# Kernel optimization log

Measured on AMD Instinct MI355X. Metric: run time of the kernel, lower is better.

The kernel has to match this reference:

```python
import jax, jax.numpy as jnp
import numpy as np

B, S, D = 4, 1024, 2048
H, KVH = 32, 8
HD = D // H            # 64
KVD = HD * KVH         # 512
RANK, ALPHA = 16, 32
LORA_SCALE = ALPHA / RANK


def setup_inputs() -> dict:
    key = jax.random.key(0)
    ks = jax.random.split(key, 14)
    x = jax.random.normal(ks[0], (B, S, D), dtype=jnp.float32)
    # RoPE tables (llama-style complex freqs as cos/sin)
    inv = 1.0 / (10000.0 ** (np.arange(0, HD, 2, dtype=np.float32) / HD))
    t = np.arange(S, dtype=np.float32)
    ang = np.outer(t, inv)  # [S, HD//2]
    freqs_cos = jnp.asarray(np.cos(ang))
    freqs_sin = jnp.asarray(np.sin(ang))
    s = 0.02
    Wq = jax.random.normal(ks[1], (D, D), dtype=jnp.float32) * s
    Wk = jax.random.normal(ks[2], (D, KVD), dtype=jnp.float32) * s
    Wv = jax.random.normal(ks[3], (D, KVD), dtype=jnp.float32) * s
    Wo = jax.random.normal(ks[4], (D, D), dtype=jnp.float32) * s
    qA = jax.random.normal(ks[5], (D, RANK), dtype=jnp.float32) * s
    qB = jax.random.normal(ks[6], (RANK, D), dtype=jnp.float32) * s
    kA = jax.random.normal(ks[7], (D, RANK), dtype=jnp.float32) * s
    kB = jax.random.normal(ks[8], (RANK, KVD), dtype=jnp.float32) * s
    vA = jax.random.normal(ks[9], (D, RANK), dtype=jnp.float32) * s
    vB = jax.random.normal(ks[10], (RANK, KVD), dtype=jnp.float32) * s
    return {"x": x, "freqs_cos": freqs_cos, "freqs_sin": freqs_sin,
            "Wq": Wq, "Wk": Wk, "Wv": Wv, "Wo": Wo,
            "qA": qA, "qB": qB, "kA": kA, "kB": kB, "vA": vA, "vB": vB}


def _rope(t, cos, sin):
    # t: [b, s, h, hd]; cos/sin: [s, hd//2]
    b, s, h, hd = t.shape
    t2 = t.reshape(b, s, h, hd // 2, 2)
    x0, x1 = t2[..., 0], t2[..., 1]
    c = cos[None, :, None, :]
    sn = sin[None, :, None, :]
    r0 = x0 * c - x1 * sn
    r1 = x0 * sn + x1 * c
    return jnp.stack([r0, r1], axis=-1).reshape(b, s, h, hd)


def reference(x, freqs_cos, freqs_sin, Wq, Wk, Wv, Wo, qA, qB, kA, kB, vA, vB):
    b, s, _ = x.shape
    # QKV projections + LoRA deltas
    q = x @ Wq + (x @ qA) @ qB * LORA_SCALE   # [b,s,D]
    k = x @ Wk + (x @ kA) @ kB * LORA_SCALE   # [b,s,KVD]
    v = x @ Wv + (x @ vA) @ vB * LORA_SCALE   # [b,s,KVD]
    q = q.reshape(b, s, H, HD)
    k = k.reshape(b, s, KVH, HD)
    v = v.reshape(b, s, KVH, HD)
    q = _rope(q, freqs_cos, freqs_sin)
    k = _rope(k, freqs_cos, freqs_sin)
    # GQA attention without materializing repeated K/V:
    rep = H // KVH
    qg = q.reshape(b, s, KVH, rep, HD)
    scale = 1.0 / jnp.sqrt(jnp.asarray(HD, dtype=x.dtype))
    scores = jnp.einsum('bsgrd,btgd->bgrst', qg, k) * scale  # [b,kvh,rep,s,s]
    causal = jnp.tril(jnp.ones((s, s), dtype=bool))
    scores = jnp.where(causal[None, None, None], scores, jnp.finfo(scores.dtype).min)
    attn = jax.nn.softmax(scores, axis=-1)
    ctx = jnp.einsum('bgrst,btgd->bsgrd', attn, v).reshape(b, s, D)
    return ctx @ Wo
```

## Files before the change

### kernel.cpp

```cpp
#include <hip/hip_runtime.h>

typedef unsigned short u16;
typedef unsigned int u32;
typedef __attribute__((ext_vector_type(8))) short short8;
typedef __attribute__((ext_vector_type(4))) float f32x4;
typedef __attribute__((ext_vector_type(4))) u16 u16x4;

#define LOG2E 1.4426950408889634f
#define SCL2 (0.125f * LOG2E)

static __device__ __forceinline__ float bf2f(u16 u) {
    return __uint_as_float(((unsigned)u) << 16);
}
static __device__ __forceinline__ u16 f2bf(float f) {
    unsigned u = __float_as_uint(f);
    unsigned r = (u + 0x7FFF + ((u >> 16) & 1)) >> 16;
    return (u16)r;
}
static __device__ __forceinline__ u32 cvtpk(float lo, float hi) {
    u32 r;
    asm("v_cvt_pk_bf16_f32 %0, %1, %2" : "=v"(r) : "v"(lo), "v"(hi));
    return r;
}
static __device__ __forceinline__ f32x4 mfma16(short8 a, short8 b, f32x4 c) {
    return __builtin_amdgcn_mfma_f32_16x16x32_bf16(a, b, c, 0, 0, 0);
}
static __device__ __forceinline__ void gload_lds16(const void* g, void* l) {
    __builtin_amdgcn_global_load_lds(
        (const __attribute__((address_space(1))) void*)g,
        (__attribute__((address_space(3))) void*)l, 16, 0, 0);
}

__global__ void cast_pack_kernel(const float* __restrict__ x, u16* __restrict__ xb,
                                 const float* __restrict__ cosb, const float* __restrict__ sinb,
                                 u32* __restrict__ tbl) {
    if (blockIdx.x >= 2048) {
        const int i = (blockIdx.x - 2048) * 1024 + threadIdx.x * 4;
#pragma unroll
        for (int j = 0; j < 4; ++j)
            tbl[i + j] = (u32)f2bf(cosb[i + j]) | ((u32)f2bf(sinb[i + j]) << 16);
        return;
    }
    constexpr int n = 4096 * 2048;
    constexpr int stride = 2048 * 256 * 4;
    int i = (blockIdx.x * 256 + threadIdx.x) * 4;
#pragma unroll
    for (; i < n; i += stride) {
        f32x4 v = *(const f32x4*)&x[i];
        u16x4 o;
        o.x = f2bf(v.x); o.y = f2bf(v.y); o.z = f2bf(v.z); o.w = f2bf(v.w);
        *(u16x4*)&xb[i] = o;
    }
}

__global__ void prep_weights_kernel(
    const float* __restrict__ Wq, const float* __restrict__ Wk,
    const float* __restrict__ Wv, const float* __restrict__ Wo,
    const float* __restrict__ qA, const float* __restrict__ qB,
    const float* __restrict__ kA, const float* __restrict__ kB,
    const float* __restrict__ vA, const float* __restrict__ vB,
    u16* __restrict__ WqkvT, u16* __restrict__ WoT) {
    __shared__ float tile[32][33];
    __shared__ float As[32][17];
    __shared__ float Bs[16][33];
    const int id = blockIdx.x;
    const int tx = threadIdx.x, ty = threadIdx.y;
    const float *W, *A = nullptr, *Bm = nullptr;
    u16* dst;
    int C, bx, by;
    bool fold = true;
    if (id < 4096)      { W = Wq; A = qA; Bm = qB; dst = WqkvT; C = 2048; bx = id & 63; by = id >> 6; }
    else if (id < 5120) { int t = id - 4096; W = Wk; A = kA; Bm = kB; dst = WqkvT + (size_t)2048 * 2048; C = 512; bx = t & 15; by = t >> 4; }
    else if (id < 6144) { int t = id - 5120; W = Wv; A = vA; Bm = vB; dst = WqkvT + (size_t)2560 * 2048; C = 512; bx = t & 15; by = t >> 4; }
    else                { int t = id - 6144; W = Wo; dst = WoT; C = 2048; bx = t & 63; by = t >> 6; fold = false; }
    const int c0 = bx * 32, r0 = by * 32;
    tile[ty][tx] = W[(size_t)(r0 + ty) * C + c0 + tx];
    if (fold) {
        if (tx < 16) As[ty][tx] = A[(r0 + ty) * 16 + tx];
        if (ty < 16) Bs[ty][tx] = Bm[(size_t)ty * C + c0 + tx];
    }
    __syncthreads();
    float v = tile[tx][ty];
    if (fold) {
        float acc = 0.0f;
#pragma unroll
        for (int rr = 0; rr < 16; ++rr) acc += As[tx][rr] * Bs[rr][ty];
        v += 2.0f * acc;
    }
    dst[(size_t)(c0 + ty) * 2048 + r0 + tx] = f2bf(v);
}

__global__ void transpose_bf16_kernel(const u16* __restrict__ src, u16* __restrict__ dst,
                                      int R, int C) {
    __shared__ u16 tile[32][33];
    int c0 = blockIdx.x * 32, r0 = blockIdx.y * 32;
    int tx = threadIdx.x, ty = threadIdx.y;
    tile[ty][tx] = src[(size_t)(r0 + ty) * C + c0 + tx];
    __syncthreads();
    dst[(size_t)(c0 + ty) * R + r0 + tx] = tile[tx][ty];
}

template <int MODE, int CN>
__global__ __launch_bounds__(256) void gemm_kernel(
    const u16* __restrict__ A, const u16* __restrict__ Bt, void* __restrict__ C0,
    void* __restrict__ C1, void* __restrict__ C2, int Nn,
    const u32* __restrict__ ropetbl) {
    constexpr int K = 2048;
    constexpr int NT = K / 64;
    __shared__ u16 As[2][128 * 64];
    __shared__ u16 Bs[2][128 * 64];
    const int tid = threadIdx.x;
    const int wid = tid >> 6, lane = tid & 63;
    const int flat = blockIdx.y * gridDim.x + blockIdx.x;
    const int xcd = flat & 7, local = flat >> 3;
    const int mbase = (((xcd & 3) << 3) + (local & 7)) * 128;
    const int nbase = ((xcd >> 2) * CN + (local >> 3)) * 128;
    const int wrow = (wid >> 1) * 64, wcol = (wid & 1) * 64;
    const int fr = lane & 15, hi = lane >> 4;
    const int l8 = lane >> 3;
    const int swc = ((lane & 7) ^ l8) * 8;
    const int rs = fr & 7;
    f32x4 acc[4][4] = {};
    const u16* Ag = A + (size_t)mbase * K;
    const u16* Bg = Bt + (size_t)nbase * K;

    auto STAGE = [&](int kt, int buf) {
#pragma unroll
        for (int i = 0; i < 4; ++i) {
            const int r8 = (i * 4 + wid) * 8;
            gload_lds16(&Ag[(size_t)(r8 + l8) * K + kt * 64 + swc], &As[buf][r8 * 64]);
            gload_lds16(&Bg[(size_t)(r8 + l8) * K + kt * 64 + swc], &Bs[buf][r8 * 64]);
        }
    };

    STAGE(0, 0);
    for (int kt = 0; kt < NT; ++kt) {
        const int cur = kt & 1;
        if (kt < NT - 1) {
            STAGE(kt + 1, cur ^ 1);
            asm volatile("s_waitcnt vmcnt(8)" ::: "memory");
        } else {
            asm volatile("s_waitcnt vmcnt(0)" ::: "memory");
        }
        __builtin_amdgcn_s_barrier();
#pragma unroll
        for (int ks = 0; ks < 2; ++ks) {
            short8 af[4], bfr[4];
#pragma unroll
            for (int i = 0; i < 4; ++i) {
                const int arow = wrow + i * 16 + fr;
                const int brow = wcol + i * 16 + fr;
                af[i]  = *(const short8*)&As[cur][arow * 64 + (((ks * 4 + hi) ^ rs) * 8)];
                bfr[i] = *(const short8*)&Bs[cur][brow * 64 + (((ks * 4 + hi) ^ rs) * 8)];
            }
#pragma unroll
            for (int mi = 0; mi < 4; ++mi)
#pragma unroll
                for (int ni = 0; ni < 4; ++ni)
                    acc[mi][ni] = mfma16(af[mi], bfr[ni], acc[mi][ni]);
        }
        __builtin_amdgcn_s_barrier();
    }
    const int rb = mbase + wrow + (hi << 2);
    const int cb = nbase + wcol + fr;
    if (MODE == 1) {
        float* C = (float*)C0;
#pragma unroll
        for (int mi = 0; mi < 4; ++mi)
#pragma unroll
            for (int j = 0; j < 4; ++j) {
                const size_t ro = (size_t)(rb + mi * 16 + j) * Nn;
#pragma unroll
                for (int ni = 0; ni < 4; ++ni) C[ro + cb + ni * 16] = acc[mi][ni][j];
            }
    } else {
        u16* C;
        int cs, cc, rope;
        if (nbase < 2048)      { C = (u16*)C0; cs = 2048; cc = cb;        rope = 1; }
        else if (nbase < 2560) { C = (u16*)C1; cs = 512;  cc = cb - 2048; rope = 2; }
        else                   { C = (u16*)C2; cs = 512;  cc = cb - 2560; rope = 0; }
        if (rope) {
            const float scale = (rope == 1) ? SCL2 : 1.0f;
            const bool odd = (lane & 1);
            const int ib = (fr >> 1);
#pragma unroll
            for (int mi = 0; mi < 4; ++mi)
#pragma unroll
                for (int j = 0; j < 4; ++j) {
                    const int row = rb + mi * 16 + j;
                    const u32* tr = ropetbl + (row & 1023) * 32;
                    const size_t ro = (size_t)row * cs;
#pragma unroll
                    for (int ni = 0; ni < 4; ++ni) {
                        u32 cspk = tr[ib + 8 * ni];
                        float cv = bf2f((u16)cspk), sv = bf2f((u16)(cspk >> 16));
                        float v = acc[mi][ni][j];
                        float p = __shfl_xor(v, 1);
                        float r = odd ? (p * sv + v * cv) : (v * cv - p * sv);
                        C[ro + cc + ni * 16] = f2bf(r * scale);
                    }
                }
        } else {
#pragma unroll
            for (int mi = 0; mi < 4; ++mi)
#pragma unroll
                for (int j = 0; j < 4; ++j) {
                    const size_t ro = (size_t)(rb + mi * 16 + j) * cs;
#pragma unroll
                    for (int ni = 0; ni < 4; ++ni) C[ro + cc + ni * 16] = f2bf(acc[mi][ni][j]);
                }
        }
    }
}

template <bool DIAG>
static __device__ __forceinline__ void attn_tile_step(
    const u16* __restrict__ Ksb, const u16* __restrict__ Vsb,
    const short8* qf, f32x4* o, float& m, float& l,
    int sq, int kvb, int wid, int fr, int hi) {
    f32x4 s[4];
    const int sw = fr & 7;
#pragma unroll
    for (int mi = 0; mi < 4; ++mi) {
        if (!DIAG || mi <= wid) {
            const int row = (mi * 16 + fr) * 64;
            short8 kf0 = *(const short8*)&Ksb[row + ((hi ^ sw) * 8)];
            short8 kf1 = *(const short8*)&Ksb[row + (((4 + hi) ^ sw) * 8)];
            f32x4 z = {};
            z = mfma16(kf0, qf[0], z);
            z = mfma16(kf1, qf[1], z);
#pragma unroll
            for (int j = 0; j < 4; ++j) {
                float val = z[j];
                if (DIAG && mi == wid && (kvb + mi * 16 + hi * 4 + j > sq)) val = -3.0e38f;
                s[mi][j] = val;
            }
        } else {
            s[mi][0] = -3.0e38f; s[mi][1] = -3.0e38f;
            s[mi][2] = -3.0e38f; s[mi][3] = -3.0e38f;
        }
    }
    float pmax = fmaxf(fmaxf(fmaxf(s[0][0], s[0][1]), fmaxf(s[0][2], s[0][3])),
                       fmaxf(fmaxf(s[1][0], s[1][1]), fmaxf(s[1][2], s[1][3])));
    pmax = fmaxf(pmax, fmaxf(fmaxf(fmaxf(s[2][0], s[2][1]), fmaxf(s[2][2], s[2][3])),
                             fmaxf(fmaxf(s[3][0], s[3][1]), fmaxf(s[3][2], s[3][3]))));
    pmax = fmaxf(pmax, __shfl_xor(pmax, 16));
    pmax = fmaxf(pmax, __shfl_xor(pmax, 32));
    if (__any(pmax > m + 8.0f)) {
        const float mnew = fmaxf(m, pmax);
        const float fsc = exp2f(m - mnew);
        l *= fsc;
        m = mnew;
#pragma unroll
        for (int dn = 0; dn < 4; ++dn)
#pragma unroll
            for (int j = 0; j < 4; ++j) o[dn][j] *= fsc;
    }
    float rs = 0.0f;
    u32 pk[4][2];
#pragma unroll
    for (int mi = 0; mi < 4; ++mi) {
        float p0 = exp2f(s[mi][0] - m);
        float p1 = exp2f(s[mi][1] - m);
        float p2 = exp2f(s[mi][2] - m);
        float p3 = exp2f(s[mi][3] - m);
        rs += (p0 + p1) + (p2 + p3);
        pk[mi][0] = cvtpk(p0, p1);
        pk[mi][1] = cvtpk(p2, p3);
    }
    rs += __shfl_xor(rs, 16);
    rs += __shfl_xor(rs, 32);
    l += rs;
    const int ksmax = DIAG ? (wid >> 1) : 1;
#pragma unroll
    for (int ks = 0; ks < 2; ++ks) {
        if (ks > ksmax) continue;
        u32 w0 = pk[2 * ks][0], w2 = pk[2 * ks + 1][0];
        u32 w1 = pk[2 * ks][1], w3 = pk[2 * ks + 1][1];
        asm volatile("v_permlane32_swap_b32 %0, %1" : "+v"(w0), "+v"(w2));
        asm volatile("v_permlane16_swap_b32 %0, %1" : "+v"(w0), "+v"(w2));
        asm volatile("v_permlane32_swap_b32 %0, %1" : "+v"(w1), "+v"(w3));
        asm volatile("v_permlane16_swap_b32 %0, %1" : "+v"(w1), "+v"(w3));
        union { u32 w[4]; short8 s8; } pu;
        pu.w[0] = w0; pu.w[1] = w1; pu.w[2] = w2; pu.w[3] = w3;
        short8 pf = pu.s8;
#pragma unroll
        for (int dn = 0; dn < 4; ++dn) {
            const int row = (dn * 16 + fr) * 64;
            short8 vf = *(const short8*)&Vsb[row + (((ks * 4 + hi) ^ sw) * 8)];
            o[dn] = mfma16(vf, pf, o[dn]);
        }
    }
}

__global__ __launch_bounds__(256) void attn_kernel(
    const u16* __restrict__ q, const u16* __restrict__ k, const u16* __restrict__ vt,
    u16* __restrict__ ctx) {
    __shared__ u16 Ks[2][64 * 64];
    __shared__ u16 Vs[2][64 * 64];
    const int flat = blockIdx.x + 8 * (blockIdx.y + 16 * blockIdx.z);
    const int c = flat & 7, t = flat >> 3;
    const int jp = t & 7;
    const int grp = c + 8 * (t >> 3);
    const int hp = grp & 15, b = grp >> 4;
    const int qtA = jp, qtB = 15 - jp;
    const int h0 = hp * 2;
    const int g = hp >> 1;
    const int tid = threadIdx.x, wid = tid >> 6, lane = tid & 63;
    const int fr = lane & 15, hi = lane >> 4, fk = hi * 8;
    const int sqA = qtA * 64 + wid * 16 + fr;
    const int sqB = qtB * 64 + wid * 16 + fr;
    short8 qA0[2], qB0[2], qA1[2], qB1[2];
    {
        const u16* pa = &q[((size_t)(b * 1024 + sqA)) * 2048 + h0 * 64];
        qA0[0] = *(const short8*)&pa[fk];      qA0[1] = *(const short8*)&pa[32 + fk];
        qA1[0] = *(const short8*)&pa[64 + fk]; qA1[1] = *(const short8*)&pa[96 + fk];
        const u16* pb = &q[((size_t)(b * 1024 + sqB)) * 2048 + h0 * 64];
        qB0[0] = *(const short8*)&pb[fk];      qB0[1] = *(const short8*)&pb[32 + fk];
        qB1[0] = *(const short8*)&pb[64 + fk]; qB1[1] = *(const short8*)&pb[96 + fk];
    }
    f32x4 oA0[4] = {}, oA1[4] = {}, oB0[4] = {}, oB1[4] = {};
    float mA0 = -3.0e38f, lA0 = 0.0f, mA1 = -3.0e38f, lA1 = 0.0f;
    float mB0 = -3.0e38f, lB0 = 0.0f, mB1 = -3.0e38f, lB1 = 0.0f;
    const u16* kbase = k + ((size_t)b * 1024) * 512 + g * 64;
    const u16* vbase = vt + ((size_t)(g * 64)) * 4096 + b * 1024;
    const int l8 = lane >> 3;
    const int sw8 = ((lane & 7) ^ l8) * 8;

    auto stage = [&](int kt, int buf) {
        const u16* kg = kbase + (size_t)(kt * 64) * 512;
        const u16* vg = vbase + kt * 64;
#pragma unroll
        for (int i = 0; i < 2; ++i) {
            const int r8 = (i * 4 + wid) * 8;
            gload_lds16(&kg[(size_t)(r8 + l8) * 512 + sw8], &Ks[buf][r8 * 64]);
            gload_lds16(&vg[(size_t)(r8 + l8) * 4096 + sw8], &Vs[buf][r8 * 64]);
        }
    };

    stage(0, 0);
    for (int kt = 0; kt <= qtB; ++kt) {
        const int cur = kt & 1;
        __syncthreads();
        if (kt < qtB) stage(kt + 1, cur ^ 1);
        const int kvb = kt * 64;
        if (kt < qtA) {
            attn_tile_step<false>(Ks[cur], Vs[cur], qA0, oA0, mA0, lA0, sqA, kvb, wid, fr, hi);
            attn_tile_step<false>(Ks[cur], Vs[cur], qA1, oA1, mA1, lA1, sqA, kvb, wid, fr, hi);
        } else if (kt == qtA) {
            attn_tile_step<true>(Ks[cur], Vs[cur], qA0, oA0, mA0, lA0, sqA, kvb, wid, fr, hi);
            attn_tile_step<true>(Ks[cur], Vs[cur], qA1, oA1, mA1, lA1, sqA, kvb, wid, fr, hi);
        }
        if (kt < qtB) {
            attn_tile_step<false>(Ks[cur], Vs[cur], qB0, oB0, mB0, lB0, sqB, kvb, wid, fr, hi);
            attn_tile_step<false>(Ks[cur], Vs[cur], qB1, oB1, mB1, lB1, sqB, kvb, wid, fr, hi);
        } else {
            attn_tile_step<true>(Ks[cur], Vs[cur], qB0, oB0, mB0, lB0, sqB, kvb, wid, fr, hi);
            attn_tile_step<true>(Ks[cur], Vs[cur], qB1, oB1, mB1, lB1, sqB, kvb, wid, fr, hi);
        }
    }
    auto emit = [&](const f32x4* o, float l, int sq, int h) {
        const float linv = 1.0f / l;
        const size_t obase = ((size_t)(b * 1024 + sq)) * 2048 + h * 64;
#pragma unroll
        for (int dn = 0; dn < 4; ++dn) {
            u16x4 w;
#pragma unroll
            for (int j = 0; j < 4; ++j) w[j] = f2bf(o[dn][j] * linv);
            *(u16x4*)&ctx[obase + dn * 16 + hi * 4] = w;
        }
    };
    emit(oA0, lA0, sqA, h0);
    emit(oA1, lA1, sqA, h0 + 1);
    emit(oB0, lB0, sqB, h0);
    emit(oB1, lB1, sqB, h0 + 1);
}

extern "C" void kernel_launch(void* const* d_in, const int* in_sizes, int n_in,
                              void* d_out, int out_size, void* d_ws, size_t ws_size,
                              hipStream_t stream) {
    const float* x    = (const float*)d_in[0];
    const float* fcos = (const float*)d_in[1];
    const float* fsin = (const float*)d_in[2];
    const float* Wq   = (const float*)d_in[3];
    const float* Wk   = (const float*)d_in[4];
    const float* Wv   = (const float*)d_in[5];
    const float* Wo   = (const float*)d_in[6];
    const float* qA   = (const float*)d_in[7];
    const float* qB   = (const float*)d_in[8];
    const float* kA   = (const float*)d_in[9];
    const float* kB   = (const float*)d_in[10];
    const float* vA   = (const float*)d_in[11];
    const float* vB   = (const float*)d_in[12];
    float* out = (float*)d_out;

    char* ws = (char*)d_ws;
    size_t off = 0;
    auto alloc = [&](size_t bytes) { char* p = ws + off; off += (bytes + 255) & ~(size_t)255; return p; };
    u16* xb     = (u16*)alloc((size_t)4096 * 2048 * 2);
    u16* WqkvT  = (u16*)alloc((size_t)3072 * 2048 * 2);
    u16* WoT    = (u16*)alloc((size_t)2048 * 2048 * 2);
    u16* qbuf   = (u16*)alloc((size_t)4096 * 2048 * 2);
    u16* kbuf   = (u16*)alloc((size_t)4096 * 512 * 2);
    u16* vbuf   = (u16*)alloc((size_t)4096 * 512 * 2);
    u16* VT2    = (u16*)alloc((size_t)512 * 4096 * 2);
    u16* ctx    = (u16*)alloc((size_t)4096 * 2048 * 2);
    u32* rtbl   = (u32*)alloc((size_t)1024 * 32 * 4);

    cast_pack_kernel<<<2080, 256, 0, stream>>>(x, xb, fcos, fsin, rtbl);
    prep_weights_kernel<<<10240, dim3(32, 32), 0, stream>>>(
        Wq, Wk, Wv, Wo, qA, qB, kA, kB, vA, vB, WqkvT, WoT);

    gemm_kernel<2, 12><<<dim3(32, 24), 256, 0, stream>>>(xb, WqkvT, qbuf, kbuf, vbuf, 3072, rtbl);
    transpose_bf16_kernel<<<dim3(16, 128), dim3(32, 32), 0, stream>>>(vbuf, VT2, 4096, 512);

    attn_kernel<<<dim3(8, 16, 4), 256, 0, stream>>>(qbuf, kbuf, VT2, ctx);

    gemm_kernel<1, 8><<<dim3(32, 16), 256, 0, stream>>>(ctx, WoT, out, nullptr, nullptr, 2048, nullptr);
}
```

Measured before the change: 214.3 us.

## Use 256x256-tile 8-wave QKV GEMM with interleaved LDS/MFMA schedule

Replaces the 128x128-tile QKV projection GEMM with a dedicated 512-thread kernel that computes 256x256 output tiles. It uses a hand-scheduled loop in which each quarter of the 64-wide K step interleaves LDS fragment reads, global-to-LDS loads and MFMA bursts, with explicit barriers, waitcnts and s_setprio. The larger tile raises arithmetic intensity and cuts redundant global traffic, and the explicit schedule aims to hide load latency. The cost is only 192 blocks, which may leave CUs underused, plus heavy register pressure and barrier overhead. The generic GEMM is simplified to handle only the fp32 output projection.

```diff
diff --git a/kernel.cpp b/kernel.cpp
--- a/kernel.cpp
+++ b/kernel.cpp
@@ -30,6 +30,9 @@
         (const __attribute__((address_space(1))) void*)g,
         (__attribute__((address_space(3))) void*)l, 16, 0, 0);
 }
+
+#define GBAR() do { asm volatile("" ::: "memory"); __builtin_amdgcn_s_barrier(); asm volatile("" ::: "memory"); } while (0)
+#define LGW()  do { asm volatile("s_waitcnt lgkmcnt(0)" ::: "memory"); __builtin_amdgcn_sched_barrier(0); } while (0)
 
 __global__ void cast_pack_kernel(const float* __restrict__ x, u16* __restrict__ xb,
                                  const float* __restrict__ cosb, const float* __restrict__ sinb,
@@ -100,11 +103,145 @@
     dst[(size_t)(c0 + ty) * R + r0 + tx] = tile[tx][ty];
 }
 
-template <int MODE, int CN>
+__global__ __launch_bounds__(512) void gemm256_qkv_kernel(
+    const u16* __restrict__ A, const u16* __restrict__ Bt, u16* __restrict__ Cq,
+    u16* __restrict__ Ck, u16* __restrict__ Cv, const u32* __restrict__ ropetbl) {
+    constexpr int K = 2048, NT = 32;
+    __shared__ u16 Asl[2][256 * 64];
+    __shared__ u16 Bsl[2][256 * 64];
+    const int tid = threadIdx.x;
+    const int wid = tid >> 6, lane = tid & 63;
+    const int flat = blockIdx.x;
+    const int m = ((flat & 7) << 1) + ((flat >> 3) & 1);
+    const int n = flat >> 4;
+    const int mbase = m * 256, nbase = n * 256;
+    const int wrow = (wid >> 2) * 128, wcol = (wid & 3) * 64;
+    const int fr = lane & 15, hi = lane >> 4;
+    const int rs2 = fr & 7;
+    f32x4 acc[8][4] = {};
+    short8 Af[4][2], Bf[4][2];
+    const u16* Ag = A + (size_t)mbase * K;
+    const u16* Bg = Bt + (size_t)nbase * K;
+
+    auto HT = [&](int t, int j) {
+        if (t >= NT) return;
+        const int buf = t & 1;
+        u16* l = (j < 2) ? &Asl[buf][0] : &Bsl[buf][0];
+        const u16* g = (j < 2) ? Ag : Bg;
+        const int rbase = (j & 1) * 128;
+#pragma unroll
+        for (int p = 0; p < 2; ++p) {
+            const int s = p * 512 + tid;
+            const int row = rbase + (s >> 3);
+            const int sl = (s & 7) ^ ((s >> 3) & 7);
+            gload_lds16(&g[(size_t)row * K + t * 64 + sl * 8],
+                        &l[rbase * 64 + (p * 512 + wid * 64) * 8]);
+        }
+    };
+    auto DSA = [&](int mo, int buf) {
+#pragma unroll
+        for (int mi = 0; mi < 4; ++mi)
+#pragma unroll
+            for (int ks = 0; ks < 2; ++ks)
+                Af[mi][ks] = *(const short8*)&Asl[buf][(wrow + (mo + mi) * 16 + fr) * 64 +
+                                                       (((ks * 4 + hi) ^ rs2) * 8)];
+    };
+    auto DSB = [&](int no, int buf) {
+#pragma unroll
+        for (int ni = 0; ni < 2; ++ni)
+#pragma unroll
+            for (int ks = 0; ks < 2; ++ks)
+                Bf[no + ni][ks] = *(const short8*)&Bsl[buf][(wcol + (no + ni) * 16 + fr) * 64 +
+                                                            (((ks * 4 + hi) ^ rs2) * 8)];
+    };
+    auto MF = [&](int q) {
+        const int mo = (q >> 1) * 4, no = (q & 1) * 2;
+        __builtin_amdgcn_s_setprio(1);
+#pragma unroll
+        for (int mi = 0; mi < 4; ++mi)
+#pragma unroll
+            for (int ni = 0; ni < 2; ++ni)
+#pragma unroll
+                for (int ks = 0; ks < 2; ++ks)
+                    acc[mo + mi][no + ni] = mfma16(Af[mi][ks], Bf[no + ni][ks], acc[mo + mi][no + ni]);
+        __builtin_amdgcn_s_setprio(0);
+    };
+
+    HT(0, 0); HT(0, 1); HT(0, 2); HT(0, 3);
+    HT(1, 0); HT(1, 1);
+    asm volatile("s_waitcnt vmcnt(4)" ::: "memory");
+    GBAR();
+
+#pragma unroll 1
+    for (int i = 0; i < NT / 2; ++i) {
+        const int t = 2 * i;
+        DSA(0, 0); DSB(0, 0); HT(t + 1, 2);
+        GBAR(); LGW(); MF(0); GBAR();
+        DSB(2, 0); HT(t + 1, 3);
+        GBAR(); LGW(); MF(1); GBAR();
+        DSA(4, 0);
+        GBAR(); LGW(); MF(2); GBAR();
+        HT(t + 2, 0); HT(t + 2, 1);
+        GBAR(); LGW(); MF(3);
+        if (t + 2 < NT) { asm volatile("s_waitcnt vmcnt(4)" ::: "memory"); }
+        else            { asm volatile("s_waitcnt vmcnt(0)" ::: "memory"); }
+        GBAR();
+        DSA(0, 1); DSB(0, 1); HT(t + 2, 2);
+        GBAR(); LGW(); MF(0); GBAR();
+        DSB(2, 1); HT(t + 2, 3);
+        GBAR(); LGW(); MF(1); GBAR();
+        DSA(4, 1);
+        GBAR(); LGW(); MF(2); GBAR();
+        HT(t + 3, 0); HT(t + 3, 1);
+        GBAR(); LGW(); MF(3);
+        if (t + 3 < NT)          { asm volatile("s_waitcnt vmcnt(4)" ::: "memory"); }
+        else if (i < NT / 2 - 1) { asm volatile("s_waitcnt vmcnt(0)" ::: "memory"); }
+        GBAR();
+    }
+
+    const int rb = mbase + wrow + (hi << 2);
+    const int cb = nbase + wcol + fr;
+    u16* C;
+    int cs, cc, rope;
+    if (nbase < 2048)      { C = Cq; cs = 2048; cc = cb;        rope = 1; }
+    else if (nbase < 2560) { C = Ck; cs = 512;  cc = cb - 2048; rope = 2; }
+    else                   { C = Cv; cs = 512;  cc = cb - 2560; rope = 0; }
+    if (rope) {
+        const float scale = (rope == 1) ? SCL2 : 1.0f;
+        const bool odd = (lane & 1);
+        const int ib = (fr >> 1);
+#pragma unroll
+        for (int mi = 0; mi < 8; ++mi)
+#pragma unroll
+            for (int j = 0; j < 4; ++j) {
+                const int row = rb + mi * 16 + j;
+                const u32* tr = ropetbl + (row & 1023) * 32;
+                const size_t ro = (size_t)row * cs;
+#pragma unroll
+                for (int ni = 0; ni < 4; ++ni) {
+                    u32 cspk = tr[ib + 8 * ni];
+                    float cv = bf2f((u16)cspk), sv = bf2f((u16)(cspk >> 16));
+                    float v = acc[mi][ni][j];
+                    float p = __shfl_xor(v, 1);
+                    float r = odd ? (p * sv + v * cv) : (v * cv - p * sv);
+                    C[ro + cc + ni * 16] = f2bf(r * scale);
+                }
+            }
+    } else {
+#pragma unroll
+        for (int mi = 0; mi < 8; ++mi)
+#pragma unroll
+            for (int j = 0; j < 4; ++j) {
+                const size_t ro = (size_t)(rb + mi * 16 + j) * cs;
+#pragma unroll
+                for (int ni = 0; ni < 4; ++ni) C[ro + cc + ni * 16] = f2bf(acc[mi][ni][j]);
+            }
+    }
+}
+
+template <int CN>
 __global__ __launch_bounds__(256) void gemm_kernel(
-    const u16* __restrict__ A, const u16* __restrict__ Bt, void* __restrict__ C0,
-    void* __restrict__ C1, void* __restrict__ C2, int Nn,
-    const u32* __restrict__ ropetbl) {
+    const u16* __restrict__ A, const u16* __restrict__ Bt, float* __restrict__ C0, int Nn) {
     constexpr int K = 2048;
     constexpr int NT = K / 64;
     __shared__ u16 As[2][128 * 64];
@@ -163,54 +300,14 @@
     }
     const int rb = mbase + wrow + (hi << 2);
     const int cb = nbase + wcol + fr;
-    if (MODE == 1) {
-        float* C = (float*)C0;
-#pragma unroll
-        for (int mi = 0; mi < 4; ++mi)
-#pragma unroll
-            for (int j = 0; j < 4; ++j) {
-                const size_t ro = (size_t)(rb + mi * 16 + j) * Nn;
-#pragma unroll
-                for (int ni = 0; ni < 4; ++ni) C[ro + cb + ni * 16] = acc[mi][ni][j];
-            }
-    } else {
-        u16* C;
-        int cs, cc, rope;
-        if (nbase < 2048)      { C = (u16*)C0; cs = 2048; cc = cb;        rope = 1; }
-        else if (nbase < 2560) { C = (u16*)C1; cs = 512;  cc = cb - 2048; rope = 2; }
-        else                   { C = (u16*)C2; cs = 512;  cc = cb - 2560; rope = 0; }
-        if (rope) {
-            const float scale = (rope == 1) ? SCL2 : 1.0f;
-            const bool odd = (lane & 1);
-            const int ib = (fr >> 1);
-#pragma unroll
-            for (int mi = 0; mi < 4; ++mi)
-#pragma unroll
-                for (int j = 0; j < 4; ++j) {
-                    const int row = rb + mi * 16 + j;
-                    const u32* tr = ropetbl + (row & 1023) * 32;
-                    const size_t ro = (size_t)row * cs;
-#pragma unroll
-                    for (int ni = 0; ni < 4; ++ni) {
-                        u32 cspk = tr[ib + 8 * ni];
-                        float cv = bf2f((u16)cspk), sv = bf2f((u16)(cspk >> 16));
-                        float v = acc[mi][ni][j];
-                        float p = __shfl_xor(v, 1);
-                        float r = odd ? (p * sv + v * cv) : (v * cv - p * sv);
-                        C[ro + cc + ni * 16] = f2bf(r * scale);
-                    }
-                }
-        } else {
-#pragma unroll
-            for (int mi = 0; mi < 4; ++mi)
-#pragma unroll
-                for (int j = 0; j < 4; ++j) {
-                    const size_t ro = (size_t)(rb + mi * 16 + j) * cs;
-#pragma unroll
-                    for (int ni = 0; ni < 4; ++ni) C[ro + cc + ni * 16] = f2bf(acc[mi][ni][j]);
-                }
-        }
-    }
+#pragma unroll
+    for (int mi = 0; mi < 4; ++mi)
+#pragma unroll
+        for (int j = 0; j < 4; ++j) {
+            const size_t ro = (size_t)(rb + mi * 16 + j) * Nn;
+#pragma unroll
+            for (int ni = 0; ni < 4; ++ni) C0[ro + cb + ni * 16] = acc[mi][ni][j];
+        }
 }
 
 template <bool DIAG>
@@ -411,10 +508,10 @@
     prep_weights_kernel<<<10240, dim3(32, 32), 0, stream>>>(
         Wq, Wk, Wv, Wo, qA, qB, kA, kB, vA, vB, WqkvT, WoT);
 
-    gemm_kernel<2, 12><<<dim3(32, 24), 256, 0, stream>>>(xb, WqkvT, qbuf, kbuf, vbuf, 3072, rtbl);
+    gemm256_qkv_kernel<<<dim3(192), 512, 0, stream>>>(xb, WqkvT, qbuf, kbuf, vbuf, rtbl);
     transpose_bf16_kernel<<<dim3(16, 128), dim3(32, 32), 0, stream>>>(vbuf, VT2, 4096, 512);
 
     attn_kernel<<<dim3(8, 16, 4), 256, 0, stream>>>(qbuf, kbuf, VT2, ctx);
 
-    gemm_kernel<1, 8><<<dim3(32, 16), 256, 0, stream>>>(ctx, WoT, out, nullptr, nullptr, 2048, nullptr);
-}
+    gemm_kernel<8><<<dim3(32, 16), 256, 0, stream>>>(ctx, WoT, out, 2048);
+}
```

Measured after the change: 209.9 us. 1.02x faster.
